# Kernel optimization log

Measured on AMD Instinct MI355X. Metric: run time of the kernel, lower is better.

The kernel has to match this reference:

```python
import jax, jax.numpy as jnp
import numpy as np
from jax.scipy.special import logsumexp

COST_GAMMA = 0.1
MIN_ZERO_GAMMA = 0.1
_CLIP = 1.0 - 1e-7


def setup_inputs() -> dict:
    key = jax.random.key(0)
    k1, k2, k3 = jax.random.split(key, 3)
    B, D, K = 65536, 128, 1024
    xs = jax.random.normal(k1, (B, D), dtype=jnp.float32)
    xs = xs / jnp.linalg.norm(xs, axis=-1, keepdims=True)  # points on sphere S^{D-1}
    mus = jax.random.normal(k2, (D, K), dtype=jnp.float32)  # prototype params (pre-projx)
    alphas = jax.random.uniform(k3, (K,), dtype=jnp.float32)
    return {"xs": xs, "mus": mus, "alphas": alphas}


def reference(xs, mus, alphas):
    # projx: project prototype columns onto the unit sphere
    mus_p = mus / jnp.linalg.norm(mus, axis=0, keepdims=True)  # [D, K]
    # sphere cost: half squared geodesic distance, cdist-like [B, K]
    ip = jnp.clip(xs @ mus_p, -_CLIP, _CLIP)
    costs = 0.5 * jnp.arccos(ip) ** 2 + alphas  # [B, K]
    # softmin over components via stable logsumexp
    F = COST_GAMMA * logsumexp(-costs / COST_GAMMA, axis=1)  # [B]
    # soft min(F, 0): logsumexp over stacked (F, 0) == logaddexp
    F = MIN_ZERO_GAMMA * jnp.logaddexp(-F / MIN_ZERO_GAMMA, 0.0)
    return F
```

## Files before the change

kernel.cpp:

```cpp
#include <hip/hip_runtime.h>
#include <hip/hip_bf16.h>


typedef __attribute__((ext_vector_type(8))) short short8;
typedef __attribute__((ext_vector_type(4))) float f32x4;

#define KP 1024
#define DD 128

__device__ __forceinline__ unsigned int f2bf(float f) {
  unsigned int u = __float_as_uint(f);
  return (u + 0x7FFFu + ((u >> 16) & 1u)) >> 16;
}

__global__ __launch_bounds__(256) void prep_kernel(
    const float* __restrict__ mus, const float* __restrict__ alphas,
    uint4* __restrict__ bsw, float* __restrict__ w) {
  __shared__ float psum[8][32];
  __shared__ float Tt[32][129];
  __shared__ float inv_s[32];
  const int t = threadIdx.x;
  const int k0 = blockIdx.x * 32;
  const int kk = t & 31, gg = t >> 5;
  float s = 0.0f;
  for (int i = 0; i < 16; ++i) {
    float v = mus[(gg * 16 + i) * KP + k0 + kk];
    s = fmaf(v, v, s);
  }
  psum[gg][kk] = s;
  __syncthreads();
  if (t < 32) {
    float tot = 0.0f;
    for (int j = 0; j < 8; ++j) tot += psum[j][t];
    inv_s[t] = rsqrtf(tot);
    w[k0 + t] = __expf(-10.0f * alphas[k0 + t]);
  }
  for (int i = 0; i < 16; ++i) {
    int e = i * 256 + t;
    Tt[e & 31][e >> 5] = mus[(e >> 5) * KP + k0 + (e & 31)];
  }
  __syncthreads();
  #pragma unroll
  for (int i = 0; i < 2; ++i) {
    int u = i * 256 + t;
    int c32 = u & 31, w0 = u >> 5;
    float inv = inv_s[c32];
    uint4 o;
    o.x = f2bf(Tt[c32][w0 * 8 + 0] * inv) | (f2bf(Tt[c32][w0 * 8 + 1] * inv) << 16);
    o.y = f2bf(Tt[c32][w0 * 8 + 2] * inv) | (f2bf(Tt[c32][w0 * 8 + 3] * inv) << 16);
    o.z = f2bf(Tt[c32][w0 * 8 + 4] * inv) | (f2bf(Tt[c32][w0 * 8 + 5] * inv) << 16);
    o.w = f2bf(Tt[c32][w0 * 8 + 6] * inv) | (f2bf(Tt[c32][w0 * 8 + 7] * inv) << 16);
    int idx = blockIdx.x * 512 + ((c32 >> 4) << 8) + ((w0 >> 2) << 6) +
              ((w0 & 3) << 4) + (c32 & 15);
    bsw[idx] = o;
  }
}

__global__ __launch_bounds__(256, 2) void main_kernel(
    const float* __restrict__ xs, const uint4* __restrict__ bsw,
    const float* __restrict__ w, float* __restrict__ out) {
  const int t = threadIdx.x;
  const int wv = t >> 6, ln = t & 63, q = ln >> 4, l15 = ln & 15;
  const int row0 = (blockIdx.x * 4 + wv) * 32;

  short8 afr[2][4];
  #pragma unroll
  for (int mt = 0; mt < 2; ++mt)
    #pragma unroll
    for (int kkk = 0; kkk < 4; ++kkk) {
      const f32x4* p = (const f32x4*)(xs +
          (size_t)(row0 + mt * 16 + l15) * DD + kkk * 32 + q * 8);
      f32x4 f0 = __builtin_nontemporal_load(p);
      f32x4 f1 = __builtin_nontemporal_load(p + 1);
      union { short8 s; uint4 u; } a;
      a.u.x = f2bf(f0.x) | (f2bf(f0.y) << 16);
      a.u.y = f2bf(f0.z) | (f2bf(f0.w) << 16);
      a.u.z = f2bf(f1.x) | (f2bf(f1.y) << 16);
      a.u.w = f2bf(f1.z) | (f2bf(f1.w) << 16);
      afr[mt][kkk] = a.s;
    }

  float sums[8];
  #pragma unroll
  for (int i = 0; i < 8; ++i) sums[i] = 0.0f;

  const uint4* bp = bsw + ln;

  short8 bA[2][4], bB[2][4];
  auto load_b = [&](short8 bf[2][4], int j) {
    #pragma unroll
    for (int nt = 0; nt < 2; ++nt)
      #pragma unroll
      for (int kkk = 0; kkk < 4; ++kkk) {
        union { short8 s; uint4 u; } tmp;
        tmp.u = bp[(j * 8 + nt * 4 + kkk) * 64];
        bf[nt][kkk] = tmp.s;
      }
  };
  auto compute = [&](short8 bf[2][4], int j) {
    float wn[2];
    wn[0] = w[j * 32 + l15];
    wn[1] = w[j * 32 + 16 + l15];
    f32x4 acc[2][2];
    #pragma unroll
    for (int mt = 0; mt < 2; ++mt)
      #pragma unroll
      for (int nt = 0; nt < 2; ++nt)
        acc[mt][nt] = (f32x4){0.f, 0.f, 0.f, 0.f};
    #pragma unroll
    for (int kkk = 0; kkk < 4; ++kkk)
      #pragma unroll
      for (int mt = 0; mt < 2; ++mt)
        #pragma unroll
        for (int nt = 0; nt < 2; ++nt)
          acc[mt][nt] = __builtin_amdgcn_mfma_f32_16x16x32_bf16(
              afr[mt][kkk], bf[nt][kkk], acc[mt][nt], 0, 0, 0);
    #pragma unroll
    for (int mt = 0; mt < 2; ++mt)
      #pragma unroll
      for (int nt = 0; nt < 2; ++nt)
        #pragma unroll
        for (int r = 0; r < 4; ++r) {
          float x = acc[mt][nt][r];
          float z = fmaxf(fmaf(x, -0.5f, 0.5f), 0.0f);
          float h = fmaf(z, -3.6067376f, -2.3449500f);
          h = fmaf(z, h, -3.2975886f);
          h = fmaf(z, h, -5.1295823f);
          h = fmaf(z, h, -9.6179669f);
          h = fmaf(z, h, -28.8539008f);
          float e = __builtin_amdgcn_exp2f(z * h);
          sums[mt * 4 + r] = fmaf(e, wn[nt], sums[mt * 4 + r]);
        }
  };

  load_b(bA, 0);
  for (int j = 0; j < 32; j += 2) {
    load_b(bB, j + 1);
    compute(bA, j);
    load_b(bA, (j + 2 < 32) ? (j + 2) : 31);
    compute(bB, j + 1);
  }

  #pragma unroll
  for (int s2 = 1; s2 < 16; s2 <<= 1)
    #pragma unroll
    for (int r = 0; r < 8; ++r) sums[r] += __shfl_xor(sums[r], s2, 64);
  if (l15 == 0) {
    #pragma unroll
    for (int mt = 0; mt < 2; ++mt)
      #pragma unroll
      for (int r = 0; r < 4; ++r)
        out[row0 + mt * 16 + q * 4 + r] =
            0.1f * log1pf(1.0f / sums[mt * 4 + r]);
  }
}

extern "C" void kernel_launch(void* const* d_in, const int* in_sizes, int n_in,
                              void* d_out, int out_size, void* d_ws, size_t ws_size,
                              hipStream_t stream) {
  const float* xs     = (const float*)d_in[0];
  const float* mus    = (const float*)d_in[1];
  const float* alphas = (const float*)d_in[2];
  float* out = (float*)d_out;

  uint4* bsw = (uint4*)d_ws;
  float* w = (float*)((char*)d_ws + 16384 * sizeof(uint4));

  prep_kernel<<<KP / 32, 256, 0, stream>>>(mus, alphas, bsw, w);
  const int B = in_sizes[0] / DD;
  main_kernel<<<B / 128, 256, 0, stream>>>(xs, bsw, w, out);
}
```

Measured before the change: 116.2 us.

## Split K dimension across waves and reduce partial sums in shared memory

Each block now handles 32 rows instead of 128, and its four waves each process a quarter of the 1024 prototypes for the same rows. The partial softmin sums are combined through shared memory before the final log1p. This launches four times as many blocks and raises the occupancy hint to 4, trading more redundant xs loads and bf16 conversions per block for more parallelism and a shorter per-wave loop. It adds a __syncthreads and a shared-memory reduction.

```diff
diff --git a/kernel.cpp b/kernel.cpp
--- a/kernel.cpp
+++ b/kernel.cpp
@@ -56,12 +56,13 @@
   }
 }
 
-__global__ __launch_bounds__(256, 2) void main_kernel(
+__global__ __launch_bounds__(256, 4) void main_kernel(
     const float* __restrict__ xs, const uint4* __restrict__ bsw,
     const float* __restrict__ w, float* __restrict__ out) {
+  __shared__ float Spart[4][32];
   const int t = threadIdx.x;
   const int wv = t >> 6, ln = t & 63, q = ln >> 4, l15 = ln & 15;
-  const int row0 = (blockIdx.x * 4 + wv) * 32;
+  const int row0 = blockIdx.x * 32;
 
   short8 afr[2][4];
   #pragma unroll
@@ -85,22 +86,23 @@
   for (int i = 0; i < 8; ++i) sums[i] = 0.0f;
 
   const uint4* bp = bsw + ln;
+  const int J0 = wv * 8;
 
   short8 bA[2][4], bB[2][4];
-  auto load_b = [&](short8 bf[2][4], int j) {
+  auto load_b = [&](short8 bf[2][4], int J) {
     #pragma unroll
     for (int nt = 0; nt < 2; ++nt)
       #pragma unroll
       for (int kkk = 0; kkk < 4; ++kkk) {
         union { short8 s; uint4 u; } tmp;
-        tmp.u = bp[(j * 8 + nt * 4 + kkk) * 64];
+        tmp.u = bp[(J * 8 + nt * 4 + kkk) * 64];
         bf[nt][kkk] = tmp.s;
       }
   };
-  auto compute = [&](short8 bf[2][4], int j) {
+  auto compute = [&](short8 bf[2][4], int J) {
     float wn[2];
-    wn[0] = w[j * 32 + l15];
-    wn[1] = w[j * 32 + 16 + l15];
+    wn[0] = w[J * 32 + l15];
+    wn[1] = w[J * 32 + 16 + l15];
     f32x4 acc[2][2];
     #pragma unroll
     for (int mt = 0; mt < 2; ++mt)
@@ -133,12 +135,13 @@
         }
   };
 
-  load_b(bA, 0);
-  for (int j = 0; j < 32; j += 2) {
-    load_b(bB, j + 1);
-    compute(bA, j);
-    load_b(bA, (j + 2 < 32) ? (j + 2) : 31);
-    compute(bB, j + 1);
+  load_b(bA, J0);
+  #pragma unroll
+  for (int j = 0; j < 8; j += 2) {
+    load_b(bB, J0 + j + 1);
+    compute(bA, J0 + j);
+    load_b(bA, (j + 2 < 8) ? (J0 + j + 2) : (J0 + 7));
+    compute(bB, J0 + j + 1);
   }
 
   #pragma unroll
@@ -150,8 +153,12 @@
     for (int mt = 0; mt < 2; ++mt)
       #pragma unroll
       for (int r = 0; r < 4; ++r)
-        out[row0 + mt * 16 + q * 4 + r] =
-            0.1f * log1pf(1.0f / sums[mt * 4 + r]);
+        Spart[wv][mt * 16 + q * 4 + r] = sums[mt * 4 + r];
+  }
+  __syncthreads();
+  if (t < 32) {
+    float s = Spart[0][t] + Spart[1][t] + Spart[2][t] + Spart[3][t];
+    out[row0 + t] = 0.1f * log1pf(1.0f / s);
   }
 }
 
@@ -168,5 +175,5 @@
 
   prep_kernel<<<KP / 32, 256, 0, stream>>>(mus, alphas, bsw, w);
   const int B = in_sizes[0] / DD;
-  main_kernel<<<B / 128, 256, 0, stream>>>(xs, bsw, w, out);
+  main_kernel<<<B / 32, 256, 0, stream>>>(xs, bsw, w, out);
 }
```

Result: slower. 175.6 us (+51.2%).
